# Optimization experiments

Measured on AMD Instinct MI355X. Metric: run time of the kernel, lower is better.

Reference implementation:

```python
import jax, jax.numpy as jnp
import numpy as np

N = 100000   # total nodes
E = 1600000  # total edges
B = 256      # graphs per batch
F_NODE, F_EDGE, H = 35, 10, 64
N_CONV = 3
IN_DIM = 2 * H + F_EDGE  # 138
EPS = 1e-5


def setup_inputs() -> dict:
    key = jax.random.key(0)
    ks = jax.random.split(key, 16)
    node_features = jax.random.normal(ks[0], (N, F_NODE), dtype=jnp.float32)
    edge_index = jax.random.randint(ks[1], (2, E), 0, N, dtype=jnp.int64)
    edge_features = jax.random.uniform(ks[2], (E, F_EDGE), dtype=jnp.float32)
    graph_index = jnp.sort(jax.random.randint(ks[3], (N,), 0, B, dtype=jnp.int64))
    s = lambda fan_in: 1.0 / np.sqrt(fan_in)
    embed_w = jax.random.uniform(ks[4], (F_NODE, H), jnp.float32, -s(F_NODE), s(F_NODE))
    embed_b = jax.random.uniform(ks[5], (H,), jnp.float32, -s(F_NODE), s(F_NODE))
    gate_w = jax.random.uniform(ks[6], (N_CONV, IN_DIM, H), jnp.float32, -s(IN_DIM), s(IN_DIM))
    gate_b = jax.random.uniform(ks[7], (N_CONV, H), jnp.float32, -s(IN_DIM), s(IN_DIM))
    cand_w = jax.random.uniform(ks[8], (N_CONV, IN_DIM, H), jnp.float32, -s(IN_DIM), s(IN_DIM))
    cand_b = jax.random.uniform(ks[9], (N_CONV, H), jnp.float32, -s(IN_DIM), s(IN_DIM))
    bn_g = jnp.ones((N_CONV, H), dtype=jnp.float32)
    bn_b = jnp.zeros((N_CONV, H), dtype=jnp.float32)
    mlp_w1 = jax.random.uniform(ks[10], (H, 128), jnp.float32, -s(H), s(H))
    mlp_b1 = jax.random.uniform(ks[11], (128,), jnp.float32, -s(H), s(H))
    mlp_w2 = jax.random.uniform(ks[12], (128, 64), jnp.float32, -s(128), s(128))
    mlp_b2 = jax.random.uniform(ks[13], (64,), jnp.float32, -s(128), s(128))
    mlp_w3 = jax.random.uniform(ks[14], (64, 1), jnp.float32, -s(64), s(64))
    mlp_b3 = jax.random.uniform(ks[15], (1,), jnp.float32, -s(64), s(64))
    return dict(node_features=node_features, edge_index=edge_index,
                edge_features=edge_features, graph_index=graph_index,
                embed_w=embed_w, embed_b=embed_b,
                gate_w=gate_w, gate_b=gate_b, cand_w=cand_w, cand_b=cand_b,
                bn_g=bn_g, bn_b=bn_b,
                mlp_w1=mlp_w1, mlp_b1=mlp_b1, mlp_w2=mlp_w2, mlp_b2=mlp_b2,
                mlp_w3=mlp_w3, mlp_b3=mlp_b3)


def _conv(h, src, dst, edge_feat, gw, gb, cw, cb, gamma, beta):
    # gather -> concat -> gated message
    z = jnp.concatenate([h[src], h[dst], edge_feat], axis=1)  # [E, 2H+F_edge]
    g = jax.nn.sigmoid(z @ gw + gb)
    c = jax.nn.softplus(z @ cw + cb)
    m = g * c
    # scatter-add onto source nodes
    agg = jax.ops.segment_sum(m, src, num_segments=h.shape[0])
    # BatchNorm1d (training-mode batch stats, biased variance)
    mu = agg.mean(axis=0)
    var = agg.var(axis=0)
    agg_bn = (agg - mu) * jax.lax.rsqrt(var + EPS) * gamma + beta
    return jax.nn.softplus(h + agg_bn)


def reference(node_features, edge_index, edge_features, graph_index,
              embed_w, embed_b, gate_w, gate_b, cand_w, cand_b, bn_g, bn_b,
              mlp_w1, mlp_b1, mlp_w2, mlp_b2, mlp_w3, mlp_b3):
    src, dst = edge_index[0], edge_index[1]
    h = node_features @ embed_w + embed_b  # [N, H]
    for i in range(N_CONV):
        h = _conv(h, src, dst, edge_features,
                  gate_w[i], gate_b[i], cand_w[i], cand_b[i], bn_g[i], bn_b[i])
    # mean pool per graph (B is static = 256)
    pooled = jax.ops.segment_sum(h, graph_index, num_segments=B)
    counts = jax.ops.segment_sum(jnp.ones((h.shape[0],), h.dtype), graph_index, num_segments=B)
    pooled = pooled / jnp.clip(counts, 1.0, None)[:, None]
    x = jax.nn.softplus(pooled @ mlp_w1 + mlp_b1)
    x = jax.nn.softplus(x @ mlp_w2 + mlp_b2)
    return (x @ mlp_w3 + mlp_b3)[:, 0]  # [B]
```

## Files before the change

### kernel.cpp

```cpp
#include <hip/hip_runtime.h>
#include <hip/hip_bf16.h>

#define NN 100000
#define EE 1600000
#define BB 256
#define F_NODE 35
#define F_EDGE 10
#define HH 64
#define IN_DIM 138
#define N_CONV 3
#define EPSBN 1e-5f
#define NB1 ((NN + 255) / 256)

#define NBLK 4000
#define NGROUPS 25
#define SUBLEN 100
#define EPB 400
#define EFSTR 12

#define HIST_BLKS (EE / 256)
#define WPREP_BLKS 240

#define LOG2E 1.442695041f
#define LN2   0.6931471806f
#define EPSADJ (EPSBN / (LN2 * LN2))

typedef _Float16 half8 __attribute__((ext_vector_type(8)));
typedef float floatx4 __attribute__((ext_vector_type(4)));

__device__ __forceinline__ float softplus_fast(float x) {
    float t = __builtin_amdgcn_exp2f(fminf(LOG2E * x, 126.0f));
    return LN2 * __builtin_amdgcn_logf(1.0f + t);
}
__device__ __forceinline__ float mpair_pre(float g2, float c2) {
    float tg = __builtin_amdgcn_exp2f(g2);
    float sig = __builtin_amdgcn_rcpf(1.0f + tg);
    float tc = __builtin_amdgcn_exp2f(fminf(c2, 126.0f));
    float l = __builtin_amdgcn_logf(1.0f + tc);
    return sig * l;
}

__global__ __launch_bounds__(256)
void histw_kernel(const int* __restrict__ src, int* __restrict__ cnt,
                  int* __restrict__ rank,
                  const float* __restrict__ gw, const float* __restrict__ cw,
                  _Float16* __restrict__ wT) {
    int bid = blockIdx.x;
    int tid = threadIdx.x;
    if (bid < HIST_BLKS) {
        int e = bid * 256 + tid;
        rank[e] = atomicAdd(&cnt[src[e]], 1);
    } else {
        int idx = (bid - HIST_BLKS) * 256 + tid;
        int k = idx % 160;
        int n = (idx / 160) & 127;
        int layer = idx / (160 * 128);
        float v = 0.f;
        if (k < IN_DIM)
            v = (n < 64) ? (-LOG2E) * gw[layer * IN_DIM * HH + k * HH + n]
                         : ( LOG2E) * cw[layer * IN_DIM * HH + k * HH + (n - 64)];
        wT[idx] = (_Float16)v;
    }
}

__global__ __launch_bounds__(256)
void scan1_kernel(int* __restrict__ cnt, int* __restrict__ bsum, int n) {
    __shared__ int ls[256];
    int t = threadIdx.x;
    int i = blockIdx.x * 256 + t;
    int v = (i < n) ? cnt[i] : 0;
    ls[t] = v;
    __syncthreads();
#pragma unroll
    for (int off = 1; off < 256; off <<= 1) {
        int add = (t >= off) ? ls[t - off] : 0;
        __syncthreads();
        ls[t] += add;
        __syncthreads();
    }
    if (i < n) cnt[i] = ls[t] - v;
    if (t == 255) bsum[blockIdx.x] = ls[255];
}

__global__ __launch_bounds__(512)
void scan2_kernel(int* __restrict__ bsum, int nb) {
    __shared__ int ls[512];
    int t = threadIdx.x;
    int v = (t < nb) ? bsum[t] : 0;
    ls[t] = v;
    __syncthreads();
#pragma unroll
    for (int off = 1; off < 512; off <<= 1) {
        int add = (t >= off) ? ls[t - off] : 0;
        __syncthreads();
        ls[t] += add;
        __syncthreads();
    }
    if (t < nb) bsum[t] = ls[t] - v;
}

__global__ __launch_bounds__(256)
void perm_kernel(const int* __restrict__ src, const int* __restrict__ rank,
                 const int* __restrict__ offs, const int* __restrict__ bsum,
                 int* __restrict__ perm) {
    int e = blockIdx.x * 256 + threadIdx.x;
    int s = src[e];
    perm[offs[s] + bsum[s >> 8] + rank[e]] = e;
}

__global__ __launch_bounds__(256)
void gather_kernel(const int* __restrict__ perm,
                   const int* __restrict__ src, const int* __restrict__ dst,
                   const float* __restrict__ ef,
                   int* __restrict__ ssorted, int2* __restrict__ sdsorted,
                   _Float16* __restrict__ ef16) {
    int pos = blockIdx.x * 256 + threadIdx.x;
    int e = perm[pos];
    int s = src[e], d = dst[e];
    ssorted[pos] = s;
    int2 sd; sd.x = s; sd.y = d;
    sdsorted[pos] = sd;
    const float2* efe = (const float2*)(ef + (size_t)e * F_EDGE);
    uint* op = (uint*)(ef16 + (size_t)pos * EFSTR);
#pragma unroll
    for (int i = 0; i < 5; i++) {
        float2 v = efe[i];
        _Float16 h0 = (_Float16)v.x;
        _Float16 h1 = (_Float16)v.y;
        op[i] = (uint)*(unsigned short*)&h0 | ((uint)*(unsigned short*)&h1 << 16);
    }
    op[5] = 0u;
}

__global__ __launch_bounds__(256)
void embed_kernel(const float* __restrict__ nf, const float* __restrict__ w,
                  const float* __restrict__ bias, _Float16* __restrict__ h16, int n) {
    __shared__ float wl[F_NODE * HH];
    int tid = threadIdx.x;
    for (int i = tid; i < F_NODE * HH; i += 256) wl[i] = w[i];
    __syncthreads();
    int idx = blockIdx.x * 256 + tid;
    int node = idx >> 6, j = idx & 63;
    if (node >= n) return;
    float acc = bias[j];
    const float* row = nf + node * F_NODE;
#pragma unroll
    for (int k = 0; k < F_NODE; k++) acc += row[k] * wl[k * HH + j];
    h16[idx] = (_Float16)acc;
}

__device__ __forceinline__ void loadA(uint4* A,
                                      const _Float16* __restrict__ h16,
                                      const _Float16* __restrict__ ef16,
                                      int s, int d, int eg, int quad) {
    const uint4* hs = (const uint4*)(h16 + (size_t)s * HH);
    const uint4* hd = (const uint4*)(h16 + (size_t)d * HH);
    A[0] = hs[quad];
    A[1] = hs[quad + 4];
    A[2] = hd[quad];
    A[3] = hd[quad + 4];
    uint4 z; z.x = z.y = z.z = z.w = 0u;
    A[4] = z;
    const _Float16* p = ef16 + (size_t)eg * EFSTR;
    if (quad == 0) {
        uint2 a = *(const uint2*)p;
        uint2 b = *(const uint2*)(p + 4);
        A[4].x = a.x; A[4].y = a.y; A[4].z = b.x; A[4].w = b.y;
    } else if (quad == 1) {
        uint2 a = *(const uint2*)(p + 8);
        A[4].x = a.x; A[4].y = a.y;
    }
}

__global__ __launch_bounds__(128, 3)
void edge_conv_mfma(const _Float16* __restrict__ h16,
                    const int* __restrict__ ssorted,
                    const int2* __restrict__ sdsorted,
                    const _Float16* __restrict__ ef16,
                    const _Float16* __restrict__ wT,
                    const float* __restrict__ gb, const float* __restrict__ cb,
                    float* __restrict__ agg) {
    int lane = threadIdx.x & 63;
    int w = threadIdx.x >> 6;
    int quad = lane >> 4, n15 = lane & 15;
    int blockE = blockIdx.x * EPB;
    int base = blockE + ((n15 >> 2) * SUBLEN) + (n15 & 3);
    int ebase_epi = blockE + quad * SUBLEN;

    int tg = 2 * w;
    half8 B[4][5];
#pragma unroll
    for (int j = 0; j < 2; j++) {
        const _Float16* wrg = wT + ((tg + j) * 16 + n15) * 160 + quad * 8;
        const _Float16* wrc = wT + ((4 + tg + j) * 16 + n15) * 160 + quad * 8;
#pragma unroll
        for (int ks = 0; ks < 5; ks++) {
            B[j][ks]     = *(const half8*)(wrg + ks * 32);
            B[2 + j][ks] = *(const half8*)(wrc + ks * 32);
        }
    }
    float gb0 = -LOG2E * gb[tg * 16 + n15], gb1 = -LOG2E * gb[(tg + 1) * 16 + n15];
    float cb0 =  LOG2E * cb[tg * 16 + n15], cb1 =  LOG2E * cb[(tg + 1) * 16 + n15];
    int colbase = tg * 16 + n15;

    int sprev = -1;
    float am0 = 0.f, am1 = 0.f;

    uint4 A[5];
    {
        int2 sd0 = sdsorted[base];
        loadA(A, h16, ef16, sd0.x, sd0.y, base, quad);
    }
    int2 sdn = sdsorted[base + 4];

    for (int g = 0; g < NGROUPS; g++) {
        int4 ss = *(const int4*)&ssorted[ebase_epi + g * 4];

        floatx4 acc[4];
        acc[0] = (floatx4){gb0, gb0, gb0, gb0};
        acc[1] = (floatx4){gb1, gb1, gb1, gb1};
        acc[2] = (floatx4){cb0, cb0, cb0, cb0};
        acc[3] = (floatx4){cb1, cb1, cb1, cb1};

#pragma unroll
        for (int ks = 0; ks < 5; ks++) {
            half8 a = __builtin_bit_cast(half8, A[ks]);
#pragma unroll
            for (int t = 0; t < 4; t++)
                acc[t] = __builtin_amdgcn_mfma_f32_16x16x32_f16(a, B[t][ks], acc[t], 0, 0, 0);
        }

        int gl = (g + 1 < NGROUPS) ? g + 1 : NGROUPS - 1;
        loadA(A, h16, ef16, sdn.x, sdn.y, base + gl * 4, quad);
        int gp = (g + 2 < NGROUPS) ? g + 2 : NGROUPS - 1;
        sdn = sdsorted[base + gp * 4];

        float mm0[4], mm1[4];
#pragma unroll
        for (int r = 0; r < 4; r++) {
            mm0[r] = mpair_pre(acc[0][r], acc[2][r]);
            mm1[r] = mpair_pre(acc[1][r], acc[3][r]);
        }
        int srr[4] = {ss.x, ss.y, ss.z, ss.w};
#pragma unroll
        for (int r = 0; r < 4; r++) {
            int sr = srr[r];
            if (sr != sprev) {
                if (sprev >= 0) {
                    float* p = agg + (size_t)sprev * HH + colbase;
                    atomicAdd(p, am0);
                    atomicAdd(p + 16, am1);
                }
                sprev = sr;
                am0 = am1 = 0.f;
            }
            am0 += mm0[r];
            am1 += mm1[r];
        }
    }
    if (sprev >= 0) {
        float* p = agg + (size_t)sprev * HH + colbase;
        atomicAdd(p, am0);
        atomicAdd(p + 16, am1);
    }
}

__global__ __launch_bounds__(256)
void bn_stats_kernel(const float* __restrict__ agg, float* __restrict__ stats, int total) {
    __shared__ float ls[256], lss[256];
    int tid = threadIdx.x;
    float s = 0.f, ss = 0.f;
    for (int idx = blockIdx.x * 256 + tid; idx < total; idx += gridDim.x * 256) {
        float v = agg[idx];
        s += v;
        ss += v * v;
    }
    ls[tid] = s;
    lss[tid] = ss;
    __syncthreads();
    if (tid < 64) {
        s = ls[tid] + ls[tid + 64] + ls[tid + 128] + ls[tid + 192];
        ss = lss[tid] + lss[tid + 64] + lss[tid + 128] + lss[tid + 192];
        atomicAdd(&stats[tid], s);
        atomicAdd(&stats[64 + tid], ss);
    }
}

__global__ __launch_bounds__(256)
void bn_update_kernel(_Float16* __restrict__ h16,
                      float* __restrict__ agg,
                      const float* __restrict__ stats,
                      const float* __restrict__ g, const float* __restrict__ b,
                      int total, float invN) {
    int idx = blockIdx.x * 256 + threadIdx.x;
    if (idx >= total) return;
    int j = idx & 63;
    float mu = stats[j] * invN;
    float var = stats[64 + j] * invN - mu * mu;
    var = fmaxf(var, 0.0f);
    float scale = g[j] * rsqrtf(var + EPSADJ);
    float a = agg[idx];
    agg[idx] = 0.f;
    float v = (float)h16[idx] + (a - mu) * scale + b[j];
    h16[idx] = (_Float16)softplus_fast(v);
}

__global__ __launch_bounds__(256)
void pool_kernel(const _Float16* __restrict__ h16, const int* __restrict__ gi,
                 float* __restrict__ pool, float* __restrict__ counts, int n) {
    int tid = threadIdx.x;
    int grp = tid >> 6;
    int j = tid & 63;
    int n0 = blockIdx.x * 64 + grp * 16;
    if (n0 >= n) return;
    int nend = n0 + 16; if (nend > n) nend = n;
    int gprev = gi[n0];
    float a = 0.f;
    int cnt = 0;
    for (int nn = n0; nn < nend; nn++) {
        int gg = gi[nn];
        if (gg != gprev) {
            atomicAdd(&pool[gprev * 64 + j], a);
            if (j == 0) atomicAdd(&counts[gprev], (float)cnt);
            a = 0.f; cnt = 0; gprev = gg;
        }
        a += (float)h16[(size_t)nn * 64 + j];
        cnt++;
    }
    atomicAdd(&pool[gprev * 64 + j], a);
    if (j == 0) atomicAdd(&counts[gprev], (float)cnt);
}

__global__ __launch_bounds__(128)
void mlp_kernel(const float* __restrict__ pool, const float* __restrict__ counts,
                const float* __restrict__ w1, const float* __restrict__ b1,
                const float* __restrict__ w2, const float* __restrict__ b2,
                const float* __restrict__ w3, const float* __restrict__ b3,
                float* __restrict__ out) {
    __shared__ float x0[64], x1[128], x2[64];
    int b = blockIdx.x, t = threadIdx.x;
    if (t < 64) {
        float c = counts[b];
        c = c < 1.f ? 1.f : c;
        x0[t] = pool[b * 64 + t] / c;
    }
    __syncthreads();
    {
        float acc = 0.f;
#pragma unroll
        for (int k = 0; k < 64; k++) acc += x0[k] * w1[k * 128 + t];
        x1[t] = softplus_fast(acc + b1[t]);
    }
    __syncthreads();
    if (t < 64) {
        float acc = 0.f;
#pragma unroll
        for (int k = 0; k < 128; k++) acc += x1[k] * w2[k * 64 + t];
        x2[t] = softplus_fast(acc + b2[t]);
    }
    __syncthreads();
    if (t == 0) {
        float acc = 0.f;
        for (int k = 0; k < 64; k++) acc += x2[k] * w3[k];
        out[b] = acc + b3[0];
    }
}

extern "C" void kernel_launch(void* const* d_in, const int* in_sizes, int n_in,
                              void* d_out, int out_size, void* d_ws, size_t ws_size,
                              hipStream_t stream) {
    const float* nf      = (const float*)d_in[0];
    const int*   ei      = (const int*)d_in[1];
    const float* ef      = (const float*)d_in[2];
    const int*   gi      = (const int*)d_in[3];
    const float* embed_w = (const float*)d_in[4];
    const float* embed_b = (const float*)d_in[5];
    const float* gate_w  = (const float*)d_in[6];
    const float* gate_b  = (const float*)d_in[7];
    const float* cand_w  = (const float*)d_in[8];
    const float* cand_b  = (const float*)d_in[9];
    const float* bn_g    = (const float*)d_in[10];
    const float* bn_b    = (const float*)d_in[11];
    const float* w1      = (const float*)d_in[12];
    const float* b1      = (const float*)d_in[13];
    const float* w2      = (const float*)d_in[14];
    const float* b2      = (const float*)d_in[15];
    const float* w3      = (const float*)d_in[16];
    const float* b3      = (const float*)d_in[17];
    float* out = (float*)d_out;

    const int NH = NN * HH;
    char* p = (char*)d_ws;
    int*       offs    = (int*)p;              p += (size_t)NN * 4;
    float*     agg     = (float*)p;            p += (size_t)NH * 4;
    float*     stats   = (float*)p;            p += 3 * 128 * 4;
    float*     pool    = (float*)p;            p += (size_t)BB * HH * 4;
    float*     counts  = (float*)p;            p += (size_t)BB * 4;
    size_t zero_bytes = (size_t)(p - (char*)d_ws);
    _Float16*  h16     = (_Float16*)p;         p += (size_t)NH * 2;
    int*       ssorted = (int*)p;              p += (size_t)EE * 4;
    int2*      sdsorted= (int2*)p;             p += (size_t)EE * 8;
    _Float16*  ef16    = (_Float16*)p;         p += (size_t)EE * EFSTR * 2;
    int*       perm    = (int*)p;              p += (size_t)EE * 4;
    int*       rank    = (int*)p;              p += (size_t)EE * 4;
    _Float16*  wTall   = (_Float16*)p;         p += (size_t)3 * 128 * 160 * 2;
    int*       bsum    = (int*)p;              p += 512 * 4;

    const int* src = ei;
    const int* dst = ei + EE;

    hipMemsetAsync(d_ws, 0, zero_bytes, stream);

    histw_kernel<<<HIST_BLKS + WPREP_BLKS, 256, 0, stream>>>(
        src, offs, rank, gate_w, cand_w, wTall);
    scan1_kernel<<<NB1, 256, 0, stream>>>(offs, bsum, NN);
    scan2_kernel<<<1, 512, 0, stream>>>(bsum, NB1);
    perm_kernel<<<EE / 256, 256, 0, stream>>>(src, rank, offs, bsum, perm);
    gather_kernel<<<EE / 256, 256, 0, stream>>>(perm, src, dst, ef, ssorted, sdsorted, ef16);

    embed_kernel<<<NH / 256, 256, 0, stream>>>(nf, embed_w, embed_b, h16, NN);

    for (int i = 0; i < N_CONV; i++) {
        edge_conv_mfma<<<NBLK, 128, 0, stream>>>(
            h16, ssorted, sdsorted, ef16,
            wTall + (size_t)i * 128 * 160,
            gate_b + i * HH, cand_b + i * HH, agg);
        bn_stats_kernel<<<512, 256, 0, stream>>>(agg, stats + i * 128, NH);
        bn_update_kernel<<<NH / 256, 256, 0, stream>>>(
            h16, agg, stats + i * 128, bn_g + i * HH, bn_b + i * HH, NH, 1.0f / (float)NN);
    }

    pool_kernel<<<(NN + 63) / 64, 256, 0, stream>>>(h16, gi, pool, counts, NN);
    mlp_kernel<<<BB, 128, 0, stream>>>(pool, counts, w1, b1, w2, b2, w3, b3, out);
}
```

Before: 832.6 us.

## Fuse prep kernels, single-pass scan, and pooling into bn update

Merges embedding, edge histogram, weight prep and graph node counting into one prep launch, and replaces the two-kernel scan with a last-block-finishes scan using atomics. Pooling is folded into the final batch-norm update via per-element atomics, removing the pool kernel. Agg gets a separate buffer per layer so it no longer needs re-zeroing, at the cost of a larger memset and heavy atomic contention on the pool buffer.

```diff
diff --git a/kernel.cpp b/kernel.cpp
--- a/kernel.cpp
+++ b/kernel.cpp
@@ -18,8 +18,11 @@
 #define EPB 400
 #define EFSTR 12
 
-#define HIST_BLKS (EE / 256)
-#define WPREP_BLKS 240
+#define PR_EMBED 25000
+#define PR_HIST  6250
+#define PR_W     240
+#define PR_NODE  NB1
+#define PR_TOT (PR_EMBED + PR_HIST + PR_W + PR_NODE)
 
 #define LOG2E 1.442695041f
 #define LN2   0.6931471806f
@@ -41,17 +44,30 @@
 }
 
 __global__ __launch_bounds__(256)
-void histw_kernel(const int* __restrict__ src, int* __restrict__ cnt,
-                  int* __restrict__ rank,
-                  const float* __restrict__ gw, const float* __restrict__ cw,
-                  _Float16* __restrict__ wT) {
+void prep_kernel(const float* __restrict__ nf, const float* __restrict__ ew,
+                 const float* __restrict__ eb, _Float16* __restrict__ h16,
+                 const int* __restrict__ src, int* __restrict__ cnt, int* __restrict__ rank,
+                 const float* __restrict__ gw, const float* __restrict__ cw,
+                 _Float16* __restrict__ wT,
+                 const int* __restrict__ gi, float* __restrict__ counts) {
     int bid = blockIdx.x;
     int tid = threadIdx.x;
-    if (bid < HIST_BLKS) {
-        int e = bid * 256 + tid;
+    if (bid < PR_EMBED) {
+        __shared__ float wl[F_NODE * HH];
+        for (int i = tid; i < F_NODE * HH; i += 256) wl[i] = ew[i];
+        __syncthreads();
+        int idx = bid * 256 + tid;
+        int node = idx >> 6, j = idx & 63;
+        float acc = eb[j];
+        const float* row = nf + node * F_NODE;
+#pragma unroll
+        for (int k = 0; k < F_NODE; k++) acc += row[k] * wl[k * HH + j];
+        h16[idx] = (_Float16)acc;
+    } else if (bid < PR_EMBED + PR_HIST) {
+        int e = (bid - PR_EMBED) * 256 + tid;
         rank[e] = atomicAdd(&cnt[src[e]], 1);
-    } else {
-        int idx = (bid - HIST_BLKS) * 256 + tid;
+    } else if (bid < PR_EMBED + PR_HIST + PR_W) {
+        int idx = (bid - PR_EMBED - PR_HIST) * 256 + tid;
         int k = idx % 160;
         int n = (idx / 160) & 127;
         int layer = idx / (160 * 128);
@@ -60,15 +76,19 @@
             v = (n < 64) ? (-LOG2E) * gw[layer * IN_DIM * HH + k * HH + n]
                          : ( LOG2E) * cw[layer * IN_DIM * HH + k * HH + (n - 64)];
         wT[idx] = (_Float16)v;
-    }
-}
-
-__global__ __launch_bounds__(256)
-void scan1_kernel(int* __restrict__ cnt, int* __restrict__ bsum, int n) {
+    } else {
+        int i = (bid - PR_EMBED - PR_HIST - PR_W) * 256 + tid;
+        if (i < NN) atomicAdd(&counts[gi[i]], 1.0f);
+    }
+}
+
+__global__ __launch_bounds__(256)
+void scan_kernel(int* __restrict__ cnt, int* __restrict__ bsum, int* __restrict__ done) {
     __shared__ int ls[256];
+    __shared__ int lastflag;
     int t = threadIdx.x;
     int i = blockIdx.x * 256 + t;
-    int v = (i < n) ? cnt[i] : 0;
+    int v = (i < NN) ? cnt[i] : 0;
     ls[t] = v;
     __syncthreads();
 #pragma unroll
@@ -78,25 +98,31 @@
         ls[t] += add;
         __syncthreads();
     }
-    if (i < n) cnt[i] = ls[t] - v;
-    if (t == 255) bsum[blockIdx.x] = ls[255];
-}
-
-__global__ __launch_bounds__(512)
-void scan2_kernel(int* __restrict__ bsum, int nb) {
-    __shared__ int ls[512];
-    int t = threadIdx.x;
-    int v = (t < nb) ? bsum[t] : 0;
-    ls[t] = v;
+    if (i < NN) cnt[i] = ls[t] - v;
+    if (t == 255)
+        __hip_atomic_store(&bsum[blockIdx.x], ls[255], __ATOMIC_RELEASE, __HIP_MEMORY_SCOPE_AGENT);
+    __syncthreads();
+    if (t == 0) {
+        int old = __hip_atomic_fetch_add(done, 1, __ATOMIC_ACQ_REL, __HIP_MEMORY_SCOPE_AGENT);
+        lastflag = (old == NB1 - 1);
+    }
+    __syncthreads();
+    if (!lastflag) return;
+    __shared__ int bs[512];
+    int v0 = (t < NB1) ? __hip_atomic_load(&bsum[t], __ATOMIC_ACQUIRE, __HIP_MEMORY_SCOPE_AGENT) : 0;
+    int v1 = (256 + t < NB1) ? __hip_atomic_load(&bsum[256 + t], __ATOMIC_ACQUIRE, __HIP_MEMORY_SCOPE_AGENT) : 0;
+    bs[t] = v0; bs[256 + t] = v1;
     __syncthreads();
 #pragma unroll
     for (int off = 1; off < 512; off <<= 1) {
-        int add = (t >= off) ? ls[t - off] : 0;
+        int a0 = bs[t];       int add0 = (t >= off) ? bs[t - off] : 0;
+        int a1 = bs[256 + t]; int add1 = (256 + t >= off) ? bs[256 + t - off] : 0;
         __syncthreads();
-        ls[t] += add;
+        bs[t] = a0 + add0; bs[256 + t] = a1 + add1;
         __syncthreads();
     }
-    if (t < nb) bsum[t] = ls[t] - v;
+    if (t < NB1) bsum[t] = (t == 0) ? 0 : bs[t - 1];
+    if (256 + t < NB1) bsum[256 + t] = bs[256 + t - 1];
 }
 
 __global__ __launch_bounds__(256)
@@ -130,23 +156,6 @@
         op[i] = (uint)*(unsigned short*)&h0 | ((uint)*(unsigned short*)&h1 << 16);
     }
     op[5] = 0u;
-}
-
-__global__ __launch_bounds__(256)
-void embed_kernel(const float* __restrict__ nf, const float* __restrict__ w,
-                  const float* __restrict__ bias, _Float16* __restrict__ h16, int n) {
-    __shared__ float wl[F_NODE * HH];
-    int tid = threadIdx.x;
-    for (int i = tid; i < F_NODE * HH; i += 256) wl[i] = w[i];
-    __syncthreads();
-    int idx = blockIdx.x * 256 + tid;
-    int node = idx >> 6, j = idx & 63;
-    if (node >= n) return;
-    float acc = bias[j];
-    const float* row = nf + node * F_NODE;
-#pragma unroll
-    for (int k = 0; k < F_NODE; k++) acc += row[k] * wl[k * HH + j];
-    h16[idx] = (_Float16)acc;
 }
 
 __device__ __forceinline__ void loadA(uint4* A,
@@ -288,47 +297,26 @@
 
 __global__ __launch_bounds__(256)
 void bn_update_kernel(_Float16* __restrict__ h16,
-                      float* __restrict__ agg,
+                      const float* __restrict__ agg,
                       const float* __restrict__ stats,
                       const float* __restrict__ g, const float* __restrict__ b,
-                      int total, float invN) {
+                      float invN, int lastlayer,
+                      const int* __restrict__ gi, float* __restrict__ pool) {
     int idx = blockIdx.x * 256 + threadIdx.x;
-    if (idx >= total) return;
     int j = idx & 63;
     float mu = stats[j] * invN;
     float var = stats[64 + j] * invN - mu * mu;
     var = fmaxf(var, 0.0f);
     float scale = g[j] * rsqrtf(var + EPSADJ);
-    float a = agg[idx];
-    agg[idx] = 0.f;
-    float v = (float)h16[idx] + (a - mu) * scale + b[j];
-    h16[idx] = (_Float16)softplus_fast(v);
-}
-
-__global__ __launch_bounds__(256)
-void pool_kernel(const _Float16* __restrict__ h16, const int* __restrict__ gi,
-                 float* __restrict__ pool, float* __restrict__ counts, int n) {
-    int tid = threadIdx.x;
-    int grp = tid >> 6;
-    int j = tid & 63;
-    int n0 = blockIdx.x * 64 + grp * 16;
-    if (n0 >= n) return;
-    int nend = n0 + 16; if (nend > n) nend = n;
-    int gprev = gi[n0];
-    float a = 0.f;
-    int cnt = 0;
-    for (int nn = n0; nn < nend; nn++) {
-        int gg = gi[nn];
-        if (gg != gprev) {
-            atomicAdd(&pool[gprev * 64 + j], a);
-            if (j == 0) atomicAdd(&counts[gprev], (float)cnt);
-            a = 0.f; cnt = 0; gprev = gg;
-        }
-        a += (float)h16[(size_t)nn * 64 + j];
-        cnt++;
-    }
-    atomicAdd(&pool[gprev * 64 + j], a);
-    if (j == 0) atomicAdd(&counts[gprev], (float)cnt);
+    float v = (float)h16[idx] + (agg[idx] - mu) * scale + b[j];
+    float hv = softplus_fast(v);
+    if (!lastlayer) {
+        h16[idx] = (_Float16)hv;
+    } else {
+        int node = idx >> 6;
+        int gg = gi[node];
+        atomicAdd(&pool[gg * 64 + j], hv);
+    }
 }
 
 __global__ __launch_bounds__(128)
@@ -392,10 +380,11 @@
     const int NH = NN * HH;
     char* p = (char*)d_ws;
     int*       offs    = (int*)p;              p += (size_t)NN * 4;
-    float*     agg     = (float*)p;            p += (size_t)NH * 4;
+    float*     agg     = (float*)p;            p += (size_t)3 * NH * 4;
     float*     stats   = (float*)p;            p += 3 * 128 * 4;
     float*     pool    = (float*)p;            p += (size_t)BB * HH * 4;
     float*     counts  = (float*)p;            p += (size_t)BB * 4;
+    int*       sync    = (int*)p;              p += 8 * 4;
     size_t zero_bytes = (size_t)(p - (char*)d_ws);
     _Float16*  h16     = (_Float16*)p;         p += (size_t)NH * 2;
     int*       ssorted = (int*)p;              p += (size_t)EE * 4;
@@ -411,25 +400,25 @@
 
     hipMemsetAsync(d_ws, 0, zero_bytes, stream);
 
-    histw_kernel<<<HIST_BLKS + WPREP_BLKS, 256, 0, stream>>>(
-        src, offs, rank, gate_w, cand_w, wTall);
-    scan1_kernel<<<NB1, 256, 0, stream>>>(offs, bsum, NN);
-    scan2_kernel<<<1, 512, 0, stream>>>(bsum, NB1);
+    prep_kernel<<<PR_TOT, 256, 0, stream>>>(
+        nf, embed_w, embed_b, h16, src, offs, rank,
+        gate_w, cand_w, wTall, gi, counts);
+
+    scan_kernel<<<NB1, 256, 0, stream>>>(offs, bsum, sync);
     perm_kernel<<<EE / 256, 256, 0, stream>>>(src, rank, offs, bsum, perm);
     gather_kernel<<<EE / 256, 256, 0, stream>>>(perm, src, dst, ef, ssorted, sdsorted, ef16);
 
-    embed_kernel<<<NH / 256, 256, 0, stream>>>(nf, embed_w, embed_b, h16, NN);
-
     for (int i = 0; i < N_CONV; i++) {
+        float* aggi = agg + (size_t)i * NH;
         edge_conv_mfma<<<NBLK, 128, 0, stream>>>(
             h16, ssorted, sdsorted, ef16,
             wTall + (size_t)i * 128 * 160,
-            gate_b + i * HH, cand_b + i * HH, agg);
-        bn_stats_kernel<<<512, 256, 0, stream>>>(agg, stats + i * 128, NH);
+            gate_b + i * HH, cand_b + i * HH, aggi);
+        bn_stats_kernel<<<512, 256, 0, stream>>>(aggi, stats + i * 128, NH);
         bn_update_kernel<<<NH / 256, 256, 0, stream>>>(
-            h16, agg, stats + i * 128, bn_g + i * HH, bn_b + i * HH, NH, 1.0f / (float)NN);
-    }
-
-    pool_kernel<<<(NN + 63) / 64, 256, 0, stream>>>(h16, gi, pool, counts, NN);
+            h16, aggi, stats + i * 128, bn_g + i * HH, bn_b + i * HH,
+            1.0f / (float)NN, (i == N_CONV - 1) ? 1 : 0, gi, pool);
+    }
+
     mlp_kernel<<<BB, 128, 0, stream>>>(pool, counts, w1, b1, w2, b2, w3, b3, out);
 }
```

After: 1.018 ms. 1.22x slower.
